# Performance work log

Measured on AMD Instinct MI355X. Metric: run time of the kernel, lower is better.

Reference implementation:

```python
import jax, jax.numpy as jnp
import numpy as np

B_, N, C = 1024, 64, 512
H = 16          # num_heads
NW = 64         # number of windows (B_ % NW == 0)


def setup_inputs() -> dict:
    key = jax.random.key(0)
    ks = jax.random.split(key, 7)
    return {
        "x": jax.random.normal(ks[0], (B_, N, C), jnp.float32),
        "mask": jax.random.normal(ks[1], (NW, N, N), jnp.float32),
        "qkv_w": jax.random.normal(ks[2], (C, 3 * C), jnp.float32) * 0.02,
        "qkv_b": jax.random.normal(ks[3], (3 * C,), jnp.float32) * 0.02,
        "proj_w": jax.random.normal(ks[4], (C, C), jnp.float32) * 0.02,
        "proj_b": jax.random.normal(ks[5], (C,), jnp.float32) * 0.02,
        "bias_table": jax.random.normal(ks[6], (2 * N - 1, H), jnp.float32) * 0.02,
    }


def reference(x, mask, qkv_w, qkv_b, proj_w, proj_b, bias_table):
    b_, n, c = x.shape
    h = bias_table.shape[1]
    ws = (bias_table.shape[0] + 1) // 2  # window_size, == n here
    d = c // h
    scale = d ** -0.5

    qkv = x @ qkv_w + qkv_b                                   # [B_, N, 3C]
    qkv = qkv.reshape(b_, n, 3, h, d).transpose(2, 0, 3, 1, 4)  # [3, B_, H, N, d]
    q, k, v = qkv[0] * scale, qkv[1], qkv[2]

    attn = jnp.einsum('bhnd,bhmd->bhnm', q, k)                # [B_, H, N, N]

    coords = jnp.arange(ws)
    rel_idx = coords[:, None] - coords[None, :] + ws - 1       # [ws, ws]
    bias = bias_table[rel_idx].transpose(2, 0, 1)              # [H, ws, ws]
    attn = attn + bias[None]

    nw = mask.shape[0]
    attn = attn.reshape(b_ // nw, nw, h, n, n) + mask[None, :, None]
    attn = attn.reshape(-1, h, n, n)
    attn = jax.nn.softmax(attn, axis=-1)

    out = jnp.einsum('bhnm,bhmd->bhnd', attn, v)               # [B_, H, N, d]
    # Faithful to the TF code: v keeps a leading singleton dim after tf.split,
    # so attn@v is [1, B_, H, N, d]; perm [0,2,1,3,4] swaps B_ and H before
    # the final reshape to (B_, N, C).
    out = out[None].transpose(0, 2, 1, 3, 4).reshape(b_, n, c)
    return out @ proj_w + proj_b
```

## Files before the change

kernel.cpp:

```cpp
#include <hip/hip_runtime.h>
#include <hip/hip_bf16.h>
#include <stdint.h>

typedef __attribute__((ext_vector_type(4))) float f32x4;
typedef __attribute__((ext_vector_type(8))) short s16x8;

__device__ __forceinline__ short f2bf(float f) {
  union { float f; uint32_t u; } v; v.f = f;
  uint32_t r = v.u + 0x7FFFu + ((v.u >> 16) & 1u);
  return (short)(r >> 16);
}

__device__ __forceinline__ void async16(const void* g, void* l) {
  __builtin_amdgcn_global_load_lds(
      (const __attribute__((address_space(1))) void*)g,
      (__attribute__((address_space(3))) void*)l, 16, 0, 0);
}

__global__ __launch_bounds__(256) void k_cast_bf16(const float* __restrict__ in,
                                                   short* __restrict__ out, int n8) {
  int i = blockIdx.x * 256 + threadIdx.x;
  if (i >= n8) return;
  const float4* p = (const float4*)in + (size_t)i * 2;
  float4 a = p[0], b = p[1];
  s16x8 o;
  o[0] = f2bf(a.x); o[1] = f2bf(a.y); o[2] = f2bf(a.z); o[3] = f2bf(a.w);
  o[4] = f2bf(b.x); o[5] = f2bf(b.y); o[6] = f2bf(b.z); o[7] = f2bf(b.w);
  ((s16x8*)out)[i] = o;
}

__global__ __launch_bounds__(256) void k_transpose_cast(const float* __restrict__ in,
                                                        short* __restrict__ out,
                                                        int K, int N) {
  int idx = blockIdx.x * 256 + threadIdx.x;
  if (idx >= K * N) return;
  int n = idx / K, k = idx - n * K;
  out[idx] = f2bf(in[(size_t)k * N + n]);
}

#define TILE_SH 16384

template <bool F32OUT>
__global__ __launch_bounds__(512, 2) void k_gemm256(const short* __restrict__ A,
                                                    const short* __restrict__ Bw,
                                                    const float* __restrict__ bias,
                                                    void* __restrict__ C,
                                                    int M, int N, int K, int nbn) {
  __shared__ short lds[2 * 2 * TILE_SH];
  const int t = threadIdx.x;
  const int w = t >> 6, l = t & 63;
  const int wm = w >> 2, wn = w & 3;

  const int nwg = gridDim.x;
  const int cpx = nwg >> 3;
  const int wg = ((int)blockIdx.x & 7) * cpx + ((int)blockIdx.x >> 3);
  const int bn = wg % nbn, bm = wg / nbn;

  const int NT = K >> 6;

  auto stage = [&](const short* __restrict__ G, int row0, int kt, short* dst) {
#pragma unroll
    for (int L = 0; L < 2; ++L) {
      int cw = L * 512 + (t & ~63);
      int c = cw + l;
      int r = c >> 3, s = c & 7;
      async16(G + (size_t)(row0 + r) * K + kt + ((s ^ (r & 7)) << 3), dst + cw * 8);
    }
  };
  auto issueA = [&](int Tt, int hf) {
    stage(A, bm * 256 + hf * 128, Tt * 64, lds + (Tt & 1) * 32768 + hf * 8192);
  };
  auto issueB = [&](int Tt, int hf) {
    stage(Bw, bn * 256 + hf * 128, Tt * 64, lds + (Tt & 1) * 32768 + TILE_SH + hf * 8192);
  };

  const int g = l >> 4, v = l & 7;
  int ofsA[2], ofsB[2];
#pragma unroll
  for (int ks = 0; ks < 2; ++ks) {
    ofsA[ks] = (wm * 128 + (l & 15)) * 64 + (((ks * 4 + g) ^ v) << 3);
    ofsB[ks] = (wn * 64 + (l & 15)) * 64 + (((ks * 4 + g) ^ v) << 3);
  }

  f32x4 acc[8][4] = {};
  s16x8 bfr[4][2];

  issueB(0, 0); issueB(0, 1); issueA(0, 0); issueA(0, 1);
  if (NT > 1) { issueB(1, 0); issueB(1, 1); }
  asm volatile("s_waitcnt vmcnt(4)" ::: "memory");
  __builtin_amdgcn_s_barrier();

#define PHASE(AI0, STAGE_STMT, TAIL_STMT)                                                                      \
  {                                                                                                            \
    s16x8 a00 = *(const s16x8*)(Ab + ofsA[0] + (AI0) * 1024);                                                  \
    s16x8 a01 = *(const s16x8*)(Ab + ofsA[1] + (AI0) * 1024);                                                  \
    s16x8 a10 = *(const s16x8*)(Ab + ofsA[0] + ((AI0) + 1) * 1024);                                            \
    s16x8 a11 = *(const s16x8*)(Ab + ofsA[1] + ((AI0) + 1) * 1024);                                            \
    STAGE_STMT;                                                                                                \
    __builtin_amdgcn_s_barrier();                                                                              \
    asm volatile("s_waitcnt lgkmcnt(0)" ::: "memory");                                                         \
    __builtin_amdgcn_s_setprio(1);                                                                             \
    _Pragma("unroll")                                                                                          \
    for (int nj = 0; nj < 4; ++nj) {                                                                           \
      acc[(AI0)][nj] = __builtin_amdgcn_mfma_f32_16x16x32_bf16(a00, bfr[nj][0], acc[(AI0)][nj], 0, 0, 0);      \
      acc[(AI0)][nj] = __builtin_amdgcn_mfma_f32_16x16x32_bf16(a01, bfr[nj][1], acc[(AI0)][nj], 0, 0, 0);      \
      acc[(AI0) + 1][nj] = __builtin_amdgcn_mfma_f32_16x16x32_bf16(a10, bfr[nj][0], acc[(AI0) + 1][nj], 0, 0, 0); \
      acc[(AI0) + 1][nj] = __builtin_amdgcn_mfma_f32_16x16x32_bf16(a11, bfr[nj][1], acc[(AI0) + 1][nj], 0, 0, 0); \
    }                                                                                                          \
    __builtin_amdgcn_s_setprio(0);                                                                             \
    TAIL_STMT;                                                                                                 \
    __builtin_amdgcn_s_barrier();                                                                              \
  }

  for (int T = 0; T < NT; ++T) {
    const short* Ab = lds + (T & 1) * 32768;
    const short* Bb = Ab + TILE_SH;
#pragma unroll
    for (int nj = 0; nj < 4; ++nj)
#pragma unroll
      for (int ks = 0; ks < 2; ++ks)
        bfr[nj][ks] = *(const s16x8*)(Bb + ofsB[ks] + nj * 1024);

    PHASE(0, if (T + 1 < NT) issueA(T + 1, 0), );
    PHASE(2, if (T + 1 < NT) issueA(T + 1, 1), );
    PHASE(4, if (T + 2 < NT) issueB(T + 2, 0), );
    PHASE(6, if (T + 2 < NT) issueB(T + 2, 1),
          if (T + 2 < NT) { asm volatile("s_waitcnt vmcnt(4)" ::: "memory"); }
          else if (T + 1 < NT) { asm volatile("s_waitcnt vmcnt(0)" ::: "memory"); });
  }
#undef PHASE

#pragma unroll
  for (int ai = 0; ai < 8; ++ai)
#pragma unroll
    for (int nj = 0; nj < 4; ++nj) {
      int col = bn * 256 + wn * 64 + nj * 16 + (l & 15);
      float bv = bias[col];
#pragma unroll
      for (int r = 0; r < 4; ++r) {
        int row = bm * 256 + wm * 128 + ai * 16 + (l >> 4) * 4 + r;
        float vv = acc[ai][nj][r] + bv;
        if (F32OUT)
          ((float*)C)[(size_t)row * N + col] = vv;
        else
          ((short*)C)[(size_t)row * N + col] = f2bf(vv);
      }
    }
}

__global__ __launch_bounds__(256) void k_attn(const short* __restrict__ qkv,
                                              const float* __restrict__ mask,
                                              const float* __restrict__ bias_table,
                                              short* __restrict__ Y) {
  __shared__ float mask_lds[64 * 64];
  __shared__ float bias_lds[4][128];
  __shared__ short p_lds[4][64][72];

  const int t = threadIdx.x, wv = t >> 6, ln = t & 63;
  const int b = blockIdx.x;
  const int h = blockIdx.y * 4 + wv;

  const float4* mk = (const float4*)(mask + (size_t)(b & 63) * 4096);
#pragma unroll
  for (int u = 0; u < 4; ++u)
    ((float4*)mask_lds)[t + 256 * u] = mk[t + 256 * u];
  for (int u = ln; u < 127; u += 64) bias_lds[wv][u] = bias_table[u * 16 + h];
  __syncthreads();

  const short* qb = qkv + (size_t)b * 64 * 1536 + h * 32;

  s16x8 qf[4], kf[4];
#pragma unroll
  for (int i = 0; i < 4; ++i) {
    qf[i] = *(const s16x8*)(qb + (size_t)(16 * i + (ln & 15)) * 1536 + (ln >> 4) * 8);
    kf[i] = *(const s16x8*)(qb + (size_t)(16 * i + (ln & 15)) * 1536 + 512 + (ln >> 4) * 8);
  }
  f32x4 s[4][4] = {};
#pragma unroll
  for (int i = 0; i < 4; ++i)
#pragma unroll
    for (int j = 0; j < 4; ++j)
      s[i][j] = __builtin_amdgcn_mfma_f32_16x16x32_bf16(qf[i], kf[j], s[i][j], 0, 0, 0);

  const float scale = 0.17677669529663687f;
  float rs[16];
#pragma unroll
  for (int i = 0; i < 4; ++i)
#pragma unroll
    for (int r = 0; r < 4; ++r) {
      int nn = 16 * i + (ln >> 4) * 4 + r;
      float vals[4];
      float vmax = -1e30f;
#pragma unroll
      for (int j = 0; j < 4; ++j) {
        int mm = 16 * j + (ln & 15);
        float x = s[i][j][r] * scale + bias_lds[wv][nn - mm + 63] + mask_lds[nn * 64 + mm];
        vals[j] = x;
        vmax = fmaxf(vmax, x);
      }
#pragma unroll
      for (int d = 1; d < 16; d <<= 1) vmax = fmaxf(vmax, __shfl_xor(vmax, d, 64));
      float sum = 0.f;
#pragma unroll
      for (int j = 0; j < 4; ++j) {
        float p = __expf(vals[j] - vmax);
        vals[j] = p;
        sum += p;
      }
#pragma unroll
      for (int d = 1; d < 16; d <<= 1) sum += __shfl_xor(sum, d, 64);
      rs[i * 4 + r] = 1.0f / sum;
#pragma unroll
      for (int j = 0; j < 4; ++j)
        p_lds[wv][nn][16 * j + (ln & 15)] = f2bf(vals[j]);
    }

  const short* vg = qb + 1024;
  f32x4 o[4][2] = {};
#pragma unroll
  for (int kk = 0; kk < 2; ++kk) {
    s16x8 pa[4];
#pragma unroll
    for (int i2 = 0; i2 < 4; ++i2)
      pa[i2] = *(const s16x8*)&p_lds[wv][16 * i2 + (ln & 15)][kk * 32 + (ln >> 4) * 8];
#pragma unroll
    for (int j2 = 0; j2 < 2; ++j2) {
      s16x8 vf;
#pragma unroll
      for (int jj = 0; jj < 8; ++jj)
        vf[jj] = vg[(size_t)(kk * 32 + (ln >> 4) * 8 + jj) * 1536 + 16 * j2 + (ln & 15)];
#pragma unroll
      for (int i2 = 0; i2 < 4; ++i2)
        o[i2][j2] = __builtin_amdgcn_mfma_f32_16x16x32_bf16(pa[i2], vf, o[i2][j2], 0, 0, 0);
    }
  }

#pragma unroll
  for (int i2 = 0; i2 < 4; ++i2)
#pragma unroll
    for (int j2 = 0; j2 < 2; ++j2)
#pragma unroll
      for (int r = 0; r < 4; ++r) {
        int n = 16 * i2 + (ln >> 4) * 4 + r;
        int d = 16 * j2 + (ln & 15);
        float val = o[i2][j2][r] * rs[i2 * 4 + r];
        int rr = h * 64 + (b >> 4);
        int ss = (b & 15) * 4 + (n >> 4);
        int cc = (n & 15) * 32 + d;
        Y[((size_t)rr * 64 + ss) * 512 + cc] = f2bf(val);
      }
}

extern "C" void kernel_launch(void* const* d_in, const int* in_sizes, int n_in,
                              void* d_out, int out_size, void* d_ws, size_t ws_size,
                              hipStream_t stream) {
  const float* x      = (const float*)d_in[0];
  const float* mask   = (const float*)d_in[1];
  const float* qkv_w  = (const float*)d_in[2];
  const float* qkv_b  = (const float*)d_in[3];
  const float* proj_w = (const float*)d_in[4];
  const float* proj_b = (const float*)d_in[5];
  const float* btab   = (const float*)d_in[6];
  float* out = (float*)d_out;

  char* w = (char*)d_ws;
  short* qkv_ws = (short*)w;
  short* xbf    = (short*)(w + (size_t)65536 * 1536 * 2);
  short* Y      = xbf;
  short* wT     = (short*)(w + (size_t)65536 * 1536 * 2 + (size_t)65536 * 512 * 2);
  short* projT  = wT + 1536 * 512;

  k_cast_bf16<<<16384, 256, 0, stream>>>(x, xbf, 33554432 / 8);
  k_transpose_cast<<<(1536 * 512 + 255) / 256, 256, 0, stream>>>(qkv_w, wT, 512, 1536);
  k_transpose_cast<<<(512 * 512 + 255) / 256, 256, 0, stream>>>(proj_w, projT, 512, 512);
  k_gemm256<false><<<1536, 512, 0, stream>>>(xbf, wT, qkv_b, qkv_ws, 65536, 1536, 512, 6);
  k_attn<<<dim3(1024, 4), 256, 0, stream>>>(qkv_ws, mask, btab, Y);
  k_gemm256<true><<<512, 512, 0, stream>>>(Y, projT, proj_b, out, 65536, 512, 512, 2);
}
```

Baseline: 307.1 us.

## Make GEMMs persistent over 256 blocks and fold softmax normalization into P

Both GEMMs now launch 256 workgroups, one per CU. Each block loops over the N-tiles of its assigned M-block, with a rotating M index per tile, and its cp.async-style pipeline runs continuously across tile boundaries so prefetch of the next tile's K-steps overlaps the epilogue. The aim is to remove wave-quantization tails and launch overhead and to keep loads in flight between tiles. In attention, the softmax reciprocal is applied to P before the bf16 cast rather than to the output, which frees the rs[] registers. The risk is that with only one block per CU, low occupancy exposes epilogue stores. Applying the reciprocal before the cast also changes rounding slightly.

```diff
diff --git a/kernel.cpp b/kernel.cpp
--- a/kernel.cpp
+++ b/kernel.cpp
@@ -41,22 +41,19 @@
 #define TILE_SH 16384
 
 template <bool F32OUT>
-__global__ __launch_bounds__(512, 2) void k_gemm256(const short* __restrict__ A,
-                                                    const short* __restrict__ Bw,
-                                                    const float* __restrict__ bias,
-                                                    void* __restrict__ C,
-                                                    int M, int N, int K, int nbn) {
+__global__ __launch_bounds__(512, 2) void k_gemm256p(const short* __restrict__ A,
+                                                     const short* __restrict__ Bw,
+                                                     const float* __restrict__ bias,
+                                                     void* __restrict__ C,
+                                                     int N, int K, int ntiles) {
   __shared__ short lds[2 * 2 * TILE_SH];
   const int t = threadIdx.x;
   const int w = t >> 6, l = t & 63;
   const int wm = w >> 2, wn = w & 3;
-
-  const int nwg = gridDim.x;
-  const int cpx = nwg >> 3;
-  const int wg = ((int)blockIdx.x & 7) * cpx + ((int)blockIdx.x >> 3);
-  const int bn = wg % nbn, bm = wg / nbn;
+  const int b = blockIdx.x;
 
   const int NT = K >> 6;
+  const int NS = ntiles * NT;
 
   auto stage = [&](const short* __restrict__ G, int row0, int kt, short* dst) {
 #pragma unroll
@@ -67,11 +64,15 @@
       async16(G + (size_t)(row0 + r) * K + kt + ((s ^ (r & 7)) << 3), dst + cw * 8);
     }
   };
-  auto issueA = [&](int Tt, int hf) {
-    stage(A, bm * 256 + hf * 128, Tt * 64, lds + (Tt & 1) * 32768 + hf * 8192);
+  auto issueA = [&](int step, int hf) {
+    int bmv = (b + step / NT) & 255;
+    int kt = step % NT;
+    stage(A, bmv * 256 + hf * 128, kt * 64, lds + (kt & 1) * 32768 + hf * 8192);
   };
-  auto issueB = [&](int Tt, int hf) {
-    stage(Bw, bn * 256 + hf * 128, Tt * 64, lds + (Tt & 1) * 32768 + TILE_SH + hf * 8192);
+  auto issueB = [&](int step, int hf) {
+    int bnv = step / NT;
+    int kt = step % NT;
+    stage(Bw, bnv * 256 + hf * 128, kt * 64, lds + (kt & 1) * 32768 + TILE_SH + hf * 8192);
   };
 
   const int g = l >> 4, v = l & 7;
@@ -86,7 +87,7 @@
   s16x8 bfr[4][2];
 
   issueB(0, 0); issueB(0, 1); issueA(0, 0); issueA(0, 1);
-  if (NT > 1) { issueB(1, 0); issueB(1, 1); }
+  issueB(1, 0); issueB(1, 1);
   asm volatile("s_waitcnt vmcnt(4)" ::: "memory");
   __builtin_amdgcn_s_barrier();
 
@@ -112,40 +113,50 @@
     __builtin_amdgcn_s_barrier();                                                                              \
   }
 
-  for (int T = 0; T < NT; ++T) {
-    const short* Ab = lds + (T & 1) * 32768;
-    const short* Bb = Ab + TILE_SH;
-#pragma unroll
-    for (int nj = 0; nj < 4; ++nj)
-#pragma unroll
-      for (int ks = 0; ks < 2; ++ks)
-        bfr[nj][ks] = *(const s16x8*)(Bb + ofsB[ks] + nj * 1024);
-
-    PHASE(0, if (T + 1 < NT) issueA(T + 1, 0), );
-    PHASE(2, if (T + 1 < NT) issueA(T + 1, 1), );
-    PHASE(4, if (T + 2 < NT) issueB(T + 2, 0), );
-    PHASE(6, if (T + 2 < NT) issueB(T + 2, 1),
-          if (T + 2 < NT) { asm volatile("s_waitcnt vmcnt(4)" ::: "memory"); }
-          else if (T + 1 < NT) { asm volatile("s_waitcnt vmcnt(0)" ::: "memory"); });
+  for (int j = 0; j < ntiles; ++j) {
+    for (int T = 0; T < NT; ++T) {
+      const int s = j * NT + T;
+      const int s1 = s + 1, s2 = s + 2;
+      const short* Ab = lds + (T & 1) * 32768;
+      const short* Bb = Ab + TILE_SH;
+#pragma unroll
+      for (int nj = 0; nj < 4; ++nj)
+#pragma unroll
+        for (int ks = 0; ks < 2; ++ks)
+          bfr[nj][ks] = *(const s16x8*)(Bb + ofsB[ks] + nj * 1024);
+
+      PHASE(0, if (s1 < NS) issueA(s1, 0), );
+      PHASE(2, if (s1 < NS) issueA(s1, 1), );
+      PHASE(4, if (s2 < NS) issueB(s2, 0), );
+      PHASE(6, if (s2 < NS) issueB(s2, 1),
+            if (s2 < NS) { asm volatile("s_waitcnt vmcnt(4)" ::: "memory"); }
+            else if (s1 < NS) { asm volatile("s_waitcnt vmcnt(0)" ::: "memory"); });
+    }
+
+    const int bmv = (b + j) & 255;
+#pragma unroll
+    for (int ai = 0; ai < 8; ++ai)
+#pragma unroll
+      for (int nj = 0; nj < 4; ++nj) {
+        int col = j * 256 + wn * 64 + nj * 16 + (l & 15);
+        float bv = bias[col];
+#pragma unroll
+        for (int r = 0; r < 4; ++r) {
+          int row = bmv * 256 + wm * 128 + ai * 16 + (l >> 4) * 4 + r;
+          float vv = acc[ai][nj][r] + bv;
+          if (F32OUT)
+            ((float*)C)[(size_t)row * N + col] = vv;
+          else
+            ((short*)C)[(size_t)row * N + col] = f2bf(vv);
+        }
+      }
+#pragma unroll
+    for (int ai = 0; ai < 8; ++ai)
+#pragma unroll
+      for (int nj = 0; nj < 4; ++nj)
+        acc[ai][nj] = (f32x4){0.f, 0.f, 0.f, 0.f};
   }
 #undef PHASE
-
-#pragma unroll
-  for (int ai = 0; ai < 8; ++ai)
-#pragma unroll
-    for (int nj = 0; nj < 4; ++nj) {
-      int col = bn * 256 + wn * 64 + nj * 16 + (l & 15);
-      float bv = bias[col];
-#pragma unroll
-      for (int r = 0; r < 4; ++r) {
-        int row = bm * 256 + wm * 128 + ai * 16 + (l >> 4) * 4 + r;
-        float vv = acc[ai][nj][r] + bv;
-        if (F32OUT)
-          ((float*)C)[(size_t)row * N + col] = vv;
-        else
-          ((short*)C)[(size_t)row * N + col] = f2bf(vv);
-      }
-    }
 }
 
 __global__ __launch_bounds__(256) void k_attn(const short* __restrict__ qkv,
@@ -183,7 +194,6 @@
       s[i][j] = __builtin_amdgcn_mfma_f32_16x16x32_bf16(qf[i], kf[j], s[i][j], 0, 0, 0);
 
   const float scale = 0.17677669529663687f;
-  float rs[16];
 #pragma unroll
   for (int i = 0; i < 4; ++i)
 #pragma unroll
@@ -209,10 +219,10 @@
       }
 #pragma unroll
       for (int d = 1; d < 16; d <<= 1) sum += __shfl_xor(sum, d, 64);
-      rs[i * 4 + r] = 1.0f / sum;
+      float rsv = 1.0f / sum;
 #pragma unroll
       for (int j = 0; j < 4; ++j)
-        p_lds[wv][nn][16 * j + (ln & 15)] = f2bf(vals[j]);
+        p_lds[wv][nn][16 * j + (ln & 15)] = f2bf(vals[j] * rsv);
     }
 
   const short* vg = qb + 1024;
@@ -243,11 +253,10 @@
       for (int r = 0; r < 4; ++r) {
         int n = 16 * i2 + (ln >> 4) * 4 + r;
         int d = 16 * j2 + (ln & 15);
-        float val = o[i2][j2][r] * rs[i2 * 4 + r];
         int rr = h * 64 + (b >> 4);
         int ss = (b & 15) * 4 + (n >> 4);
         int cc = (n & 15) * 32 + d;
-        Y[((size_t)rr * 64 + ss) * 512 + cc] = f2bf(val);
+        Y[((size_t)rr * 64 + ss) * 512 + cc] = f2bf(o[i2][j2][r]);
       }
 }
 
@@ -273,7 +282,7 @@
   k_cast_bf16<<<16384, 256, 0, stream>>>(x, xbf, 33554432 / 8);
   k_transpose_cast<<<(1536 * 512 + 255) / 256, 256, 0, stream>>>(qkv_w, wT, 512, 1536);
   k_transpose_cast<<<(512 * 512 + 255) / 256, 256, 0, stream>>>(proj_w, projT, 512, 512);
-  k_gemm256<false><<<1536, 512, 0, stream>>>(xbf, wT, qkv_b, qkv_ws, 65536, 1536, 512, 6);
+  k_gemm256p<false><<<256, 512, 0, stream>>>(xbf, wT, qkv_b, qkv_ws, 1536, 512, 6);
   k_attn<<<dim3(1024, 4), 256, 0, stream>>>(qkv_ws, mask, btab, Y);
-  k_gemm256<true><<<512, 512, 0, stream>>>(Y, projT, proj_b, out, 65536, 512, 512, 2);
-}
+  k_gemm256p<true><<<256, 512, 0, stream>>>(Y, projT, proj_b, out, 512, 512, 2);
+}
```

Result: slower. 322.0 us (+4.8%).
